# Optimization experiments

Measured on AMD Instinct MI355X. Metric: run time of the kernel, lower is better.

The kernel has to match this reference:

```python
import jax, jax.numpy as jnp
import numpy as np

N_NODES = 100000
N_EDGES = 1600000
N_GRAPHS = 256


def setup_inputs() -> dict:
    key = jax.random.key(0)
    ks = jax.random.split(key, 7)
    x = jax.random.normal(ks[0], (N_NODES, 128), dtype=jnp.float32)
    W1 = jax.random.normal(ks[1], (128, 64), dtype=jnp.float32) * (1.0 / np.sqrt(128))
    W2 = jax.random.normal(ks[2], (64, 64), dtype=jnp.float32) * (1.0 / np.sqrt(64))
    W3 = jax.random.normal(ks[3], (64, 64), dtype=jnp.float32) * (1.0 / np.sqrt(64))
    Wlin = jax.random.normal(ks[4], (64, 16), dtype=jnp.float32) * (1.0 / np.sqrt(64))
    edge_index = jax.random.randint(ks[5], (2, N_EDGES), 0, N_NODES, dtype=jnp.int64)
    batch = jnp.sort(jax.random.randint(ks[6], (N_NODES,), 0, N_GRAPHS, dtype=jnp.int64))
    return {"x": x, "W1": W1, "W2": W2, "W3": W3, "Wlin": Wlin,
            "edge_index": edge_index, "batch": batch}


def _gcn_conv(h, W, src, dst):
    # GCNConv(bias=False, normalize=False): scatter-add of transformed src feats onto dst
    m = h @ W                                   # [N, d_out]
    return jax.ops.segment_sum(m[src], dst, num_segments=N_NODES)


def reference(x, W1, W2, W3, Wlin, edge_index, batch):
    src, dst = edge_index[0], edge_index[1]
    h = jax.nn.relu(_gcn_conv(x, W1, src, dst))
    h = jax.nn.relu(_gcn_conv(h, W2, src, dst))
    h = _gcn_conv(h, W3, src, dst)
    # global mean pool over graphs
    sums = jax.ops.segment_sum(h, batch, num_segments=N_GRAPHS)      # [G, d]
    counts = jax.ops.segment_sum(jnp.ones((N_NODES,), h.dtype), batch,
                                 num_segments=N_GRAPHS)              # [G]
    pooled = sums / jnp.maximum(counts, 1.0)[:, None]
    return pooled @ Wlin                                             # [G, out]
```

## Files before the change

kernel.cpp:

```cpp
#include <hip/hip_runtime.h>
#include <hip/hip_bf16.h>

#define SCAN_CHUNK 1024
#define BIN_CHUNK  4096
#define BSH        9
#define BCAP       10240
#define GSLOTS     16
#define KNODES     2
#define GS16       32
#define GSPLIT     2

typedef __attribute__((ext_vector_type(8))) short short8v;
typedef __attribute__((ext_vector_type(4))) float f32x4;

__device__ __forceinline__ unsigned short f2bf(float f) {
    union { float f; unsigned int i; } c;
    c.f = f;
    unsigned int r = c.i + 0x7FFFu + ((c.i >> 16) & 1u);
    return (unsigned short)(r >> 16);
}
__device__ __forceinline__ float lo2f(unsigned int u) {
    union { unsigned int i; float f; } c; c.i = u << 16; return c.f;
}
__device__ __forceinline__ float hi2f(unsigned int u) {
    union { unsigned int i; float f; } c; c.i = u & 0xFFFF0000u; return c.f;
}
__device__ __forceinline__ unsigned int pack2bf(float lo, float hi) {
    return ((unsigned int)f2bf(hi) << 16) | (unsigned int)f2bf(lo);
}
__device__ __forceinline__ int idx_at(const void* p, long long i, int is64) {
    if (is64) return (int)((const long long*)p)[i];
    return ((const int*)p)[i];
}
__device__ __forceinline__ short8v as_s8(uint4 q) {
    return __builtin_bit_cast(short8v, q);
}

__global__ __launch_bounds__(256) void k_setup(const unsigned int* __restrict__ a, long long aWords,
                                               const unsigned int* __restrict__ b, long long bWords,
                                               int* __restrict__ flags, int* __restrict__ bcur,
                                               float* __restrict__ T, int tN,
                                               const float* __restrict__ W1, const float* __restrict__ W2,
                                               const float* __restrict__ W3, const float* __restrict__ Wlin,
                                               float* __restrict__ Wc,
                                               unsigned short* __restrict__ Wt1hi, unsigned short* __restrict__ Wt1lo,
                                               unsigned short* __restrict__ Wt2hi, unsigned short* __restrict__ Wt2lo,
                                               unsigned short* __restrict__ Wcthi, unsigned short* __restrict__ Wctlo) {
    int t = threadIdx.x;
    if (blockIdx.x == 0) {
        __shared__ int sA, sB;
        if (t == 0) { sA = 1; sB = 1; }
        __syncthreads();
        long long hA = aWords / 2;
        long long pA = 2 * ((long long)t * (hA - 1) / 255) + 1;
        if (a[pA] != 0u) atomicAnd(&sA, 0);
        long long hB = bWords / 2;
        long long pB = 2 * ((long long)t * (hB - 1) / 255) + 1;
        if (b[pB] != 0u) atomicAnd(&sB, 0);
        __syncthreads();
        if (t == 0) { flags[0] = sA; flags[1] = sB; }
    } else if (blockIdx.x == 1) {
        bcur[t] = 0;
        for (int o = t; o < 64 * 16; o += 256) {
            int k = o >> 4, j = o & 15;
            float acc = 0.f;
#pragma unroll 8
            for (int m = 0; m < 64; ++m) acc += W3[k * 64 + m] * Wlin[m * 16 + j];
            Wc[o] = acc;
            unsigned short h = f2bf(acc);
            Wcthi[j * 64 + k] = h;
            Wctlo[j * 64 + k] = f2bf(acc - lo2f(h));
        }
    } else if (blockIdx.x == 2) {
        int col = t >> 2, ks = (t & 3) * 32;
        for (int k = ks; k < ks + 32; ++k) {
            float v = W1[(size_t)k * 64 + col];
            unsigned short h = f2bf(v);
            Wt1hi[col * 128 + k] = h;
            Wt1lo[col * 128 + k] = f2bf(v - lo2f(h));
        }
    } else if (blockIdx.x == 3) {
        int col = t >> 2, ks = (t & 3) * 16;
        for (int k = ks; k < ks + 16; ++k) {
            float v = W2[(size_t)k * 64 + col];
            unsigned short h = f2bf(v);
            Wt2hi[col * 64 + k] = h;
            Wt2lo[col * 64 + k] = f2bf(v - lo2f(h));
        }
    } else {
        int i = (blockIdx.x - 4) * 256 + t;
        if (i < tN) T[i] = 0.f;
    }
}

__global__ __launch_bounds__(256) void k_bin(const void* __restrict__ ei, int nE,
                                             int* __restrict__ bcur, unsigned int* __restrict__ srcsE,
                                             const int* __restrict__ flags) {
    __shared__ int eS[BIN_CHUNK], eD[BIN_CHUNK];
    __shared__ int cntD[256], baseD[256], posD[256];
    int t = threadIdx.x;
    int is64 = flags[0];
    cntD[t] = 0; posD[t] = 0;
    __syncthreads();
    int cs = blockIdx.x * BIN_CHUNK;
    int ce = min(cs + BIN_CHUNK, nE);
    for (int i = cs + t; i < ce; i += 256) {
        int src = idx_at(ei, i, is64);
        int dst = idx_at(ei, (long long)nE + i, is64);
        eS[i - cs] = src; eD[i - cs] = dst;
        atomicAdd(&cntD[dst >> BSH], 1);
    }
    __syncthreads();
    if (cntD[t] > 0) baseD[t] = atomicAdd(&bcur[t], cntD[t]);
    __syncthreads();
    for (int i = cs + t; i < ce; i += 256) {
        int src = eS[i - cs], dst = eD[i - cs];
        int kd = dst >> BSH;
        int od = baseD[kd] + atomicAdd(&posD[kd], 1);
        if (od < BCAP)
            srcsE[(size_t)kd * BCAP + od] = (unsigned int)src | ((unsigned int)(dst & 511) << 17);
    }
}

__global__ __launch_bounds__(256) void k_fill3(unsigned int* __restrict__ srcsE,
                                               const int* __restrict__ bcur,
                                               int* __restrict__ rowstart, int* __restrict__ rowend,
                                               int N, const void* __restrict__ batch,
                                               const int* __restrict__ flags) {
    __shared__ unsigned int ent[BCAP];
    __shared__ int cnt5[512], off5[512], cur5[512], s2[256];
    __shared__ int grelS[512];
    __shared__ int sgf;
    int k = blockIdx.x;
    int t = threadIdx.x;
    int base = k * BCAP;
    int ck = min(bcur[k], BCAP);
    int is64b = flags[1];
    cnt5[t] = 0; cnt5[t + 256] = 0;
    if (t == 0) sgf = idx_at(batch, (long long)(k << BSH), is64b);
    __syncthreads();
    for (int i = t; i < ck; i += 256) {
        unsigned int v = srcsE[base + i];
        ent[i] = v;
        atomicAdd(&cnt5[v >> 17], 1);
    }
    __syncthreads();
    int pair = cnt5[2 * t] + cnt5[2 * t + 1];
    s2[t] = pair;
    __syncthreads();
    for (int off = 1; off < 256; off <<= 1) {
        int x = (t >= off) ? s2[t - off] : 0;
        __syncthreads();
        s2[t] += x;
        __syncthreads();
    }
    int excl = s2[t] - pair;
    off5[2 * t] = excl;
    off5[2 * t + 1] = excl + cnt5[2 * t];
    __syncthreads();
    for (int j = t; j < 512; j += 256) {
        int node = (k << BSH) + j;
        if (node < N) {
            rowstart[node] = base + off5[j];
            rowend[node]   = base + off5[j] + cnt5[j];
            grelS[j] = idx_at(batch, node, is64b) - sgf;
        } else {
            grelS[j] = 0;
        }
        cur5[j] = off5[j];
    }
    __syncthreads();
    for (int i = t; i < ck; i += 256) {
        unsigned int v = ent[i];
        int d = (int)(v >> 17);
        int pos = atomicAdd(&cur5[d], 1);
        srcsE[base + pos] = (v & 0x1FFFFu) | ((unsigned int)grelS[d] << 17);
    }
}

__global__ __launch_bounds__(256) void k_zero_i(int* __restrict__ p, int n) {
    int i = blockIdx.x * 256 + threadIdx.x;
    if (i < n) p[i] = 0;
}
__global__ __launch_bounds__(256) void k_hist(const void* __restrict__ ei, int nE,
                                              int* __restrict__ cnt, const int* __restrict__ flags) {
    int e = blockIdx.x * 256 + threadIdx.x;
    if (e >= nE) return;
    int is64 = flags[0];
    atomicAdd(&cnt[idx_at(ei, (long long)nE + e, is64)], 1);
}
__global__ __launch_bounds__(256) void k_scan_a(const int* __restrict__ cnt, int N, int* __restrict__ bsum) {
    __shared__ int s[256];
    int b = blockIdx.x, t = threadIdx.x;
    int base = b * SCAN_CHUNK + t * 4;
    int v = 0;
#pragma unroll
    for (int j = 0; j < 4; ++j) if (base + j < N) v += cnt[base + j];
    s[t] = v; __syncthreads();
    for (int off = 128; off >= 1; off >>= 1) {
        if (t < off) s[t] += s[t + off];
        __syncthreads();
    }
    if (t == 0) bsum[b] = s[0];
}
__global__ __launch_bounds__(128) void k_scan_b(const int* __restrict__ bsum, int NB, int* __restrict__ bpre) {
    __shared__ int s[128];
    int t = threadIdx.x;
    int v = (t < NB) ? bsum[t] : 0;
    s[t] = v; __syncthreads();
    for (int off = 1; off < 128; off <<= 1) {
        int x = (t >= off) ? s[t - off] : 0;
        __syncthreads();
        s[t] += x;
        __syncthreads();
    }
    if (t < NB) bpre[t] = s[t] - v;
}
__global__ __launch_bounds__(256) void k_scan_c(const int* __restrict__ cnt, int N,
                                                const int* __restrict__ bpre,
                                                int* __restrict__ rowstart, int* __restrict__ rowend,
                                                int* __restrict__ cursor) {
    __shared__ int s[256];
    int b = blockIdx.x, t = threadIdx.x;
    int base = b * SCAN_CHUNK + t * 4;
    int c0 = (base + 0 < N) ? cnt[base + 0] : 0;
    int c1 = (base + 1 < N) ? cnt[base + 1] : 0;
    int c2 = (base + 2 < N) ? cnt[base + 2] : 0;
    int c3 = (base + 3 < N) ? cnt[base + 3] : 0;
    int p0 = c0, p1 = p0 + c1, p2 = p1 + c2, p3 = p2 + c3;
    s[t] = p3; __syncthreads();
    int tot = p3;
    for (int off = 1; off < 256; off <<= 1) {
        int x = (t >= off) ? s[t - off] : 0;
        __syncthreads();
        s[t] += x;
        __syncthreads();
    }
    int toff = s[t] - tot + bpre[b];
    if (base + 0 < N) { rowstart[base + 0] = toff;      rowend[base + 0] = toff + p0; cursor[base + 0] = toff; }
    if (base + 1 < N) { rowstart[base + 1] = toff + p0; rowend[base + 1] = toff + p1; cursor[base + 1] = toff + p0; }
    if (base + 2 < N) { rowstart[base + 2] = toff + p1; rowend[base + 2] = toff + p2; cursor[base + 2] = toff + p1; }
    if (base + 3 < N) { rowstart[base + 3] = toff + p2; rowend[base + 3] = toff + p3; cursor[base + 3] = toff + p2; }
}
__global__ __launch_bounds__(256) void k_fill(const void* __restrict__ ei, int nE,
                                              int* __restrict__ cursor, int* __restrict__ srcs,
                                              const int* __restrict__ flags) {
    int e = blockIdx.x * 256 + threadIdx.x;
    if (e >= nE) return;
    int is64 = flags[0];
    int src = idx_at(ei, e, is64);
    int dst = idx_at(ei, (long long)nE + e, is64);
    int pos = atomicAdd(&cursor[dst], 1);
    srcs[pos] = src;
}

__global__ __launch_bounds__(256) void k_gemm1m(const float* __restrict__ X,
                                                const unsigned short* __restrict__ Wthi,
                                                const unsigned short* __restrict__ Wtlo,
                                                unsigned short* __restrict__ Mb, int N) {
    __shared__ unsigned short Xhi[64 * 128];
    __shared__ unsigned short Xlo[64 * 128];
    int tid = threadIdx.x;
    int wid = tid >> 6, lane = tid & 63;
    int lrow = lane & 15, lk = lane >> 4;
    int base = blockIdx.x * 64;

    uint4 bhi[4], blo[4];
    {
        int col = wid * 16 + lrow;
        const unsigned short* ph = Wthi + col * 128 + lk * 8;
        const unsigned short* pl = Wtlo + col * 128 + lk * 8;
#pragma unroll
        for (int kc = 0; kc < 4; ++kc) {
            bhi[kc] = *(const uint4*)(ph + kc * 32);
            blo[kc] = *(const uint4*)(pl + kc * 32);
        }
    }

    {
        int r = tid >> 2, seg = tid & 3;
        int row = base + r;
        float v[32];
        if (row < N) {
            const float4* src = (const float4*)(X + (size_t)row * 128 + seg * 32);
#pragma unroll
            for (int u = 0; u < 8; ++u) {
                float4 f = src[u];
                v[4 * u] = f.x; v[4 * u + 1] = f.y; v[4 * u + 2] = f.z; v[4 * u + 3] = f.w;
            }
        } else {
#pragma unroll
            for (int u = 0; u < 32; ++u) v[u] = 0.f;
        }
        int swz = (r & 7) << 4;
#pragma unroll
        for (int u = 0; u < 4; ++u) {
            unsigned short h[8];
            float lo[8];
#pragma unroll
            for (int j = 0; j < 8; ++j) {
                float xv = v[u * 8 + j];
                unsigned short hh = f2bf(xv);
                h[j] = hh;
                lo[j] = xv - lo2f(hh);
            }
            uint4 qh, ql;
            qh.x = ((unsigned)h[1] << 16) | h[0]; qh.y = ((unsigned)h[3] << 16) | h[2];
            qh.z = ((unsigned)h[5] << 16) | h[4]; qh.w = ((unsigned)h[7] << 16) | h[6];
            ql.x = pack2bf(lo[0], lo[1]); ql.y = pack2bf(lo[2], lo[3]);
            ql.z = pack2bf(lo[4], lo[5]); ql.w = pack2bf(lo[6], lo[7]);
            int kb = seg * 64 + u * 16;
            int addr = r * 256 + (kb ^ swz);
            *(uint4*)((char*)Xhi + addr) = qh;
            *(uint4*)((char*)Xlo + addr) = ql;
        }
    }
    __syncthreads();

    int col = wid * 16 + lrow;
#pragma unroll
    for (int rt = 0; rt < 4; ++rt) {
        f32x4 acc = {0.f, 0.f, 0.f, 0.f};
        int row = rt * 16 + lrow;
        int rbase = row * 256;
        int swz = (row & 7) << 4;
#pragma unroll
        for (int kc = 0; kc < 4; ++kc) {
            int kb = kc * 64 + lk * 16;
            uint4 ah = *(const uint4*)((const char*)Xhi + rbase + (kb ^ swz));
            uint4 al = *(const uint4*)((const char*)Xlo + rbase + (kb ^ swz));
            acc = __builtin_amdgcn_mfma_f32_16x16x32_bf16(as_s8(ah), as_s8(bhi[kc]), acc, 0, 0, 0);
            acc = __builtin_amdgcn_mfma_f32_16x16x32_bf16(as_s8(al), as_s8(bhi[kc]), acc, 0, 0, 0);
            acc = __builtin_amdgcn_mfma_f32_16x16x32_bf16(as_s8(ah), as_s8(blo[kc]), acc, 0, 0, 0);
        }
#pragma unroll
        for (int j = 0; j < 4; ++j) {
            int orow = base + rt * 16 + lk * 4 + j;
            if (orow < N) Mb[(size_t)orow * 64 + col] = f2bf(acc[j]);
        }
    }
}

__global__ __launch_bounds__(256) void k_projm(const unsigned short* __restrict__ Rb,
                                               const unsigned short* __restrict__ Wthi,
                                               const unsigned short* __restrict__ Wtlo,
                                               unsigned short* __restrict__ Mout, int N) {
    __shared__ unsigned short Rs[64 * 64];
    int tid = threadIdx.x;
    int wid = tid >> 6, lane = tid & 63;
    int lrow = lane & 15, lk = lane >> 4;
    int base = blockIdx.x * 64;

    uint4 bhi[2], blo[2];
    {
        int col = wid * 16 + lrow;
        const unsigned short* ph = Wthi + col * 64 + lk * 8;
        const unsigned short* pl = Wtlo + col * 64 + lk * 8;
#pragma unroll
        for (int kc = 0; kc < 2; ++kc) {
            bhi[kc] = *(const uint4*)(ph + kc * 32);
            blo[kc] = *(const uint4*)(pl + kc * 32);
        }
    }
    {
        int r = tid >> 2, seg = tid & 3;
        int row = base + r;
        uint4 q0, q1;
        if (row < N) {
            const uint4* src = (const uint4*)(Rb + (size_t)row * 64 + seg * 16);
            q0 = src[0]; q1 = src[1];
        } else {
            q0 = make_uint4(0u, 0u, 0u, 0u); q1 = q0;
        }
        int swz = (r & 7) << 4;
        int kb = seg * 32;
        *(uint4*)((char*)Rs + r * 128 + ((kb) ^ swz)) = q0;
        *(uint4*)((char*)Rs + r * 128 + ((kb + 16) ^ swz)) = q1;
    }
    __syncthreads();

    int col = wid * 16 + lrow;
#pragma unroll
    for (int rt = 0; rt < 4; ++rt) {
        f32x4 acc = {0.f, 0.f, 0.f, 0.f};
        int row = rt * 16 + lrow;
        int rbase = row * 128;
        int swz = (row & 7) << 4;
#pragma unroll
        for (int kc = 0; kc < 2; ++kc) {
            int kb = kc * 64 + lk * 16;
            uint4 a = *(const uint4*)((const char*)Rs + rbase + (kb ^ swz));
            acc = __builtin_amdgcn_mfma_f32_16x16x32_bf16(as_s8(a), as_s8(bhi[kc]), acc, 0, 0, 0);
            acc = __builtin_amdgcn_mfma_f32_16x16x32_bf16(as_s8(a), as_s8(blo[kc]), acc, 0, 0, 0);
        }
#pragma unroll
        for (int j = 0; j < 4; ++j) {
            int orow = base + rt * 16 + lk * 4 + j;
            if (orow < N) Mout[(size_t)orow * 64 + col] = f2bf(acc[j]);
        }
    }
}

__global__ __launch_bounds__(256) void k_y2(const unsigned short* __restrict__ R,
                                            const unsigned short* __restrict__ Wcthi,
                                            const unsigned short* __restrict__ Wctlo,
                                            unsigned short* __restrict__ Y2, int N) {
    int tid = threadIdx.x;
    int wid = tid >> 6, lane = tid & 63;
    int lrow = lane & 15, lk = lane >> 4;
    int rowb = blockIdx.x * 64 + wid * 16;

    uint4 bhi[2], blo[2];
#pragma unroll
    for (int kc = 0; kc < 2; ++kc) {
        bhi[kc] = *(const uint4*)(Wcthi + lrow * 64 + kc * 32 + lk * 8);
        blo[kc] = *(const uint4*)(Wctlo + lrow * 64 + kc * 32 + lk * 8);
    }
    f32x4 acc = {0.f, 0.f, 0.f, 0.f};
    int arow = rowb + lrow;
#pragma unroll
    for (int kc = 0; kc < 2; ++kc) {
        uint4 a = make_uint4(0u, 0u, 0u, 0u);
        if (arow < N) a = *(const uint4*)(R + (size_t)arow * 64 + kc * 32 + lk * 8);
        acc = __builtin_amdgcn_mfma_f32_16x16x32_bf16(as_s8(a), as_s8(bhi[kc]), acc, 0, 0, 0);
        acc = __builtin_amdgcn_mfma_f32_16x16x32_bf16(as_s8(a), as_s8(blo[kc]), acc, 0, 0, 0);
    }
#pragma unroll
    for (int j = 0; j < 4; ++j) {
        int orow = rowb + lk * 4 + j;
        if (orow < N) Y2[(size_t)orow * 16 + lrow] = f2bf(acc[j]);
    }
}

#define GACC(P)  { A[0] += lo2f((P).x); A[1] += hi2f((P).x);                  \
                   A[2] += lo2f((P).y); A[3] += hi2f((P).y);                  \
                   A[4] += lo2f((P).z); A[5] += hi2f((P).z);                  \
                   A[6] += lo2f((P).w); A[7] += hi2f((P).w); }
#define GATHER8_CORE(SRCS, MB, S, E, LMASK, L, A, MASK)                       \
    {                                                                         \
        int c_ = (S);                                                         \
        for (; c_ + 16 <= (E); c_ += 16) {                                    \
            int sv0_ = (int)(SRCS)[c_ + (L)];                                 \
            int sv1_ = (int)(SRCS)[c_ + 8 + (L)];                             \
            _Pragma("unroll")                                                 \
            for (int j_ = 0; j_ < 8; ++j_) {                                  \
                int srcn_ = __shfl(sv0_, (LMASK) | j_, 64) & (int)(MASK);     \
                uint4 p_ = ((const uint4*)((MB) + (size_t)srcn_ * 64))[L];    \
                GACC(p_)                                                      \
            }                                                                 \
            _Pragma("unroll")                                                 \
            for (int j_ = 0; j_ < 8; ++j_) {                                  \
                int srcn_ = __shfl(sv1_, (LMASK) | j_, 64) & (int)(MASK);     \
                uint4 p_ = ((const uint4*)((MB) + (size_t)srcn_ * 64))[L];    \
                GACC(p_)                                                      \
            }                                                                 \
        }                                                                     \
        if (c_ + 8 <= (E)) {                                                  \
            int sv_ = (int)(SRCS)[c_ + (L)];                                  \
            _Pragma("unroll")                                                 \
            for (int j_ = 0; j_ < 8; ++j_) {                                  \
                int srcn_ = __shfl(sv_, (LMASK) | j_, 64) & (int)(MASK);      \
                uint4 p_ = ((const uint4*)((MB) + (size_t)srcn_ * 64))[L];    \
                GACC(p_)                                                      \
            }                                                                 \
            c_ += 8;                                                          \
        }                                                                     \
        if (c_ < (E)) {                                                       \
            int m_ = (E) - c_;                                                \
            int sv_ = (int)(SRCS)[(c_ + (L) < (E)) ? c_ + (L) : (E) - 1];     \
            _Pragma("unroll")                                                 \
            for (int j_ = 0; j_ < 8; ++j_) {                                  \
                if (j_ < m_) {                                                \
                    int srcn_ = __shfl(sv_, (LMASK) | j_, 64) & (int)(MASK);  \
                    uint4 p_ = ((const uint4*)((MB) + (size_t)srcn_ * 64))[L];\
                    GACC(p_)                                                  \
                }                                                             \
            }                                                                 \
        }                                                                     \
    }

__global__ __launch_bounds__(256) void k_gather8(const unsigned short* __restrict__ Mb,
                                                 const int* __restrict__ rowstart,
                                                 const int* __restrict__ rowend,
                                                 const unsigned int* __restrict__ srcs,
                                                 unsigned short* __restrict__ R, int N,
                                                 unsigned int srcMask) {
    int tid = threadIdx.x;
    int lane = tid & 63;
    int l = lane & 7;
    int lmask = lane & 56;
    int node0 = (blockIdx.x * 32 + (tid >> 3)) * KNODES;
#pragma unroll
    for (int jn = 0; jn < KNODES; ++jn) {
        int node = node0 + jn;
        if (node >= N) break;
        int s = rowstart[node], e = rowend[node];
        float A[8] = {0.f, 0.f, 0.f, 0.f, 0.f, 0.f, 0.f, 0.f};
        GATHER8_CORE(srcs, Mb, s, e, lmask, l, A, srcMask)
        uint4 q;
        q.x = pack2bf(fmaxf(A[0], 0.f), fmaxf(A[1], 0.f));
        q.y = pack2bf(fmaxf(A[2], 0.f), fmaxf(A[3], 0.f));
        q.z = pack2bf(fmaxf(A[4], 0.f), fmaxf(A[5], 0.f));
        q.w = pack2bf(fmaxf(A[6], 0.f), fmaxf(A[7], 0.f));
        ((uint4*)(R + (size_t)node * 64))[l] = q;
    }
}

__global__ __launch_bounds__(256) void k_gsum16(const unsigned short* __restrict__ y2,
                                                const unsigned int* __restrict__ srcsE,
                                                const int* __restrict__ bcur,
                                                const void* __restrict__ batch,
                                                float* __restrict__ T16, int N, int G,
                                                const int* __restrict__ flags) {
    __shared__ float sacc[GS16][4][16];
    __shared__ int sgmin;
    int t = threadIdx.x;
    int k = blockIdx.x / GSPLIT;
    int half = blockIdx.x % GSPLIT;
    for (int i = t; i < GS16 * 4 * 16; i += 256) ((float*)sacc)[i] = 0.f;
    if (t == 0) sgmin = idx_at(batch, (long long)min(k << BSH, N - 1), flags[1]);
    __syncthreads();
    int gmin = sgmin;
    int ck = min(bcur[k], BCAP);
    int base = k * BCAP;
    int lo = half * (ck / GSPLIT);
    int hi = (half == GSPLIT - 1) ? ck : (half + 1) * (ck / GSPLIT);
    int cnt = hi - lo;
    int len = (cnt + 255) >> 8;
    int s0 = lo + t * len;
    int e0 = min(s0 + len, hi);
    int rep = t & 3;

    float acc[16];
#pragma unroll
    for (int j = 0; j < 16; ++j) acc[j] = 0.f;
    int curg = -1;

#define GF16(GG)                                                              \
    {                                                                         \
        if ((GG) < GS16) {                                                    \
            float* sp_ = &sacc[GG][rep][0];                                   \
            _Pragma("unroll")                                                 \
            for (int j_ = 0; j_ < 16; ++j_) atomicAdd(&sp_[j_], acc[j_]);     \
        } else {                                                              \
            _Pragma("unroll")                                                 \
            for (int j_ = 0; j_ < 16; ++j_)                                   \
                atomicAdd(&T16[(size_t)(gmin + (GG)) * 16 + j_], acc[j_]);    \
        }                                                                     \
    }

    int i = s0;
    while (i < e0) {
        if (i + 4 <= e0) {
            unsigned v0 = srcsE[base + i], v1 = srcsE[base + i + 1];
            unsigned v2 = srcsE[base + i + 2], v3 = srcsE[base + i + 3];
            int g0 = (int)(v0 >> 17);
            if (g0 == curg && (int)(v3 >> 17) == g0 &&
                (int)(v1 >> 17) == g0 && (int)(v2 >> 17) == g0) {
                const uint4* p0 = (const uint4*)(y2 + (size_t)(v0 & 0x1FFFFu) * 16);
                const uint4* p1 = (const uint4*)(y2 + (size_t)(v1 & 0x1FFFFu) * 16);
                const uint4* p2 = (const uint4*)(y2 + (size_t)(v2 & 0x1FFFFu) * 16);
                const uint4* p3 = (const uint4*)(y2 + (size_t)(v3 & 0x1FFFFu) * 16);
                uint4 a0 = p0[0], b0 = p0[1];
                uint4 a1 = p1[0], b1 = p1[1];
                uint4 a2 = p2[0], b2 = p2[1];
                uint4 a3 = p3[0], b3 = p3[1];
#define Y2ACC(QA, QB)                                                         \
                acc[0] += lo2f((QA).x); acc[1] += hi2f((QA).x);               \
                acc[2] += lo2f((QA).y); acc[3] += hi2f((QA).y);               \
                acc[4] += lo2f((QA).z); acc[5] += hi2f((QA).z);               \
                acc[6] += lo2f((QA).w); acc[7] += hi2f((QA).w);               \
                acc[8] += lo2f((QB).x); acc[9] += hi2f((QB).x);               \
                acc[10] += lo2f((QB).y); acc[11] += hi2f((QB).y);             \
                acc[12] += lo2f((QB).z); acc[13] += hi2f((QB).z);             \
                acc[14] += lo2f((QB).w); acc[15] += hi2f((QB).w);
                Y2ACC(a0, b0) Y2ACC(a1, b1) Y2ACC(a2, b2) Y2ACC(a3, b3)
                i += 4;
                continue;
            }
        }
        unsigned v = srcsE[base + i];
        int g = (int)(v >> 17);
        if (g != curg) {
            if (curg >= 0) GF16(curg)
            curg = g;
#pragma unroll
            for (int j = 0; j < 16; ++j) acc[j] = 0.f;
        }
        const uint4* p = (const uint4*)(y2 + (size_t)(v & 0x1FFFFu) * 16);
        uint4 qa = p[0], qb = p[1];
        Y2ACC(qa, qb)
        ++i;
    }
    if (curg >= 0) GF16(curg)
    __syncthreads();
    for (int i2 = t; i2 < GS16 * 16; i2 += 256) {
        int slot = i2 >> 4, j = i2 & 15;
        float v = sacc[slot][0][j] + sacc[slot][1][j] + sacc[slot][2][j] + sacc[slot][3][j];
        int g = gmin + slot;
        if (v != 0.f && g < G) atomicAdd(&T16[(size_t)g * 16 + j], v);
    }
#undef Y2ACC
#undef GF16
}

#define GFLUSH(GG, RR)                                                        \
    {                                                                         \
        int slot_ = (GG) - gmin;                                              \
        if (slot_ >= 0 && slot_ < GSLOTS) {                                   \
            _Pragma("unroll")                                                 \
            for (int i_ = 0; i_ < 8; ++i_)                                    \
                atomicAdd(&sacc[slot_][l * 8 + i_], RR[i_]);                  \
        } else {                                                              \
            _Pragma("unroll")                                                 \
            for (int i_ = 0; i_ < 8; ++i_)                                    \
                atomicAdd(&T[(GG) * 64 + l * 8 + i_], RR[i_]);                \
        }                                                                     \
    }

__global__ __launch_bounds__(256) void k_gsum8(const unsigned short* __restrict__ R,
                                               const int* __restrict__ rowstart,
                                               const int* __restrict__ rowend,
                                               const unsigned int* __restrict__ srcs,
                                               const void* __restrict__ batch,
                                               float* __restrict__ T, int N, int G,
                                               const int* __restrict__ flags) {
    __shared__ float sacc[GSLOTS][64];
    int tid = threadIdx.x;
    for (int t = tid; t < GSLOTS * 64; t += 256) ((float*)sacc)[t] = 0.f;
    int is64 = flags[1];
    int nbase = blockIdx.x * 32 * KNODES;
    int gmin = idx_at(batch, min(nbase, N - 1), is64);
    __syncthreads();

    int lane = tid & 63;
    int l = lane & 7;
    int lmask = lane & 56;
    int node0 = nbase + (tid >> 3) * KNODES;
    float r[8] = {0.f, 0.f, 0.f, 0.f, 0.f, 0.f, 0.f, 0.f};
    int curG = -1;
#pragma unroll
    for (int jn = 0; jn < KNODES; ++jn) {
        int node = node0 + jn;
        if (node >= N) break;
        int s = rowstart[node], e = rowend[node];
        float A[8] = {0.f, 0.f, 0.f, 0.f, 0.f, 0.f, 0.f, 0.f};
        GATHER8_CORE(srcs, R, s, e, lmask, l, A, 0xFFFFFFFFu)
        int g = idx_at(batch, node, is64);
        if (g != curG) {
            if (curG >= 0) GFLUSH(curG, r)
#pragma unroll
            for (int i = 0; i < 8; ++i) r[i] = A[i];
            curG = g;
        } else {
#pragma unroll
            for (int i = 0; i < 8; ++i) r[i] += A[i];
        }
    }
    if (curG >= 0) GFLUSH(curG, r)
    __syncthreads();
    for (int t = tid; t < GSLOTS * 64; t += 256) {
        float v = ((float*)sacc)[t];
        int g = gmin + (t >> 6);
        if (v != 0.f && g < G) atomicAdd(&T[g * 64 + (t & 63)], v);
    }
}

__global__ __launch_bounds__(64) void k_out(const float* __restrict__ T,
                                            const void* __restrict__ batch,
                                            const float* __restrict__ Wc,
                                            float* __restrict__ out, int N,
                                            const int* __restrict__ flags) {
    int g = blockIdx.x;
    int lane = threadIdx.x;
    int is64 = flags[1];

    int lo = 0, hi = N;
    while (lo < hi) { int mid = (lo + hi) >> 1; if (idx_at(batch, mid, is64) < g) lo = mid + 1; else hi = mid; }
    int s = lo;
    lo = s; hi = N;
    while (lo < hi) { int mid = (lo + hi) >> 1; if (idx_at(batch, mid, is64) < g + 1) lo = mid + 1; else hi = mid; }
    float cnt = (float)(lo - s);

    __shared__ float P[64];
    P[lane] = T[g * 64 + lane] / fmaxf(cnt, 1.0f);
    __syncthreads();
    if (lane < 16) {
        float o = 0.f;
#pragma unroll 8
        for (int k = 0; k < 64; ++k) o += P[k] * Wc[k * 16 + lane];
        out[g * 16 + lane] = o;
    }
}

__global__ __launch_bounds__(64) void k_out16(const float* __restrict__ T16,
                                              const void* __restrict__ batch,
                                              float* __restrict__ out, int N,
                                              const int* __restrict__ flags) {
    int g = blockIdx.x;
    int lane = threadIdx.x;
    int is64 = flags[1];

    int lo = 0, hi = N;
    while (lo < hi) { int mid = (lo + hi) >> 1; if (idx_at(batch, mid, is64) < g) lo = mid + 1; else hi = mid; }
    int s = lo;
    lo = s; hi = N;
    while (lo < hi) { int mid = (lo + hi) >> 1; if (idx_at(batch, mid, is64) < g + 1) lo = mid + 1; else hi = mid; }
    float cnt = (float)(lo - s);

    if (lane < 16) out[g * 16 + lane] = T16[(size_t)g * 16 + lane] / fmaxf(cnt, 1.0f);
}

extern "C" void kernel_launch(void* const* d_in, const int* in_sizes, int n_in,
                              void* d_out, int out_size, void* d_ws, size_t ws_size,
                              hipStream_t stream) {
    const float* x    = (const float*)d_in[0];
    const float* W1   = (const float*)d_in[1];
    const float* W2   = (const float*)d_in[2];
    const float* W3   = (const float*)d_in[3];
    const float* Wlin = (const float*)d_in[4];
    const void* ei    = d_in[5];
    const void* batch = d_in[6];

    int N  = in_sizes[0] / 128;
    int nE = in_sizes[5] / 2;
    int G  = out_size / 16;
    int NBUCK = (N + (1 << BSH) - 1) >> BSH;
    int NB = (N + SCAN_CHUNK - 1) / SCAN_CHUNK;
    bool fast = (NBUCK <= 256);

    unsigned short* MbA = (unsigned short*)d_ws;
    unsigned short* MbB = (unsigned short*)(MbA + (size_t)N * 64);
    int* ip       = (int*)(MbB + (size_t)N * 64);
    int* rowstart = ip;          ip += N;
    int* rowend   = ip;          ip += N;
    int* cnt      = ip;          ip += N;
    int* bsum     = ip;          ip += 128;
    int* bpre     = ip;          ip += 128;
    int* flags    = ip;          ip += 4;
    int* bcur     = ip;          ip += 256;
    float* T      = (float*)ip;  ip += (size_t)G * 64;
    float* Wc     = (float*)ip;  ip += 64 * 16;
    unsigned short* Wt1hi = (unsigned short*)ip; ip += 2048;
    ip += 2048;
    unsigned short* Wt1lo = (unsigned short*)ip; ip += 4096;
    unsigned short* Wt2hi = (unsigned short*)ip; ip += 2048;
    unsigned short* Wt2lo = (unsigned short*)ip; ip += 2048;
    unsigned short* Wcthi = (unsigned short*)ip; ip += 512;
    unsigned short* Wctlo = (unsigned short*)ip; ip += 512;
    unsigned short* Y2    = (unsigned short*)ip; ip += (size_t)N * 8;
    unsigned int* srcsE = (unsigned int*)ip;
    ip += fast ? (size_t)256 * BCAP : (size_t)nE;
    size_t need = (size_t)((char*)ip - (char*)d_ws);
    if (ws_size < need) return;

    dim3 blk(256);
    int gT64  = (N + 63) / 64;
    int gG8   = (N + 32 * KNODES - 1) / (32 * KNODES);
    int gBin  = (nE + BIN_CHUNK - 1) / BIN_CHUNK;
    int tN    = G * 64;
    int gSetup = 4 + (tN + 255) / 256;

    hipLaunchKernelGGL(k_setup, dim3(gSetup), blk, 0, stream,
                       (const unsigned int*)ei, (long long)in_sizes[5],
                       (const unsigned int*)batch, (long long)in_sizes[6],
                       flags, bcur, T, tN, W1, W2, W3, Wlin, Wc,
                       Wt1hi, Wt1lo, Wt2hi, Wt2lo, Wcthi, Wctlo);

    if (fast) {
        hipLaunchKernelGGL(k_bin,   dim3(gBin), blk, 0, stream, ei, nE, bcur, srcsE, flags);
        hipLaunchKernelGGL(k_fill3, dim3(NBUCK), blk, 0, stream, srcsE, bcur, rowstart, rowend, N, batch, flags);
    } else {
        int gN = (N + 255) / 256;
        int gE = (nE + 255) / 256;
        hipLaunchKernelGGL(k_zero_i, dim3(gN), blk, 0, stream, cnt, N);
        hipLaunchKernelGGL(k_hist,   dim3(gE), blk, 0, stream, ei, nE, cnt, flags);
        hipLaunchKernelGGL(k_scan_a, dim3(NB), blk, 0, stream, cnt, N, bsum);
        hipLaunchKernelGGL(k_scan_b, dim3(1), dim3(128), 0, stream, bsum, NB, bpre);
        hipLaunchKernelGGL(k_scan_c, dim3(NB), blk, 0, stream, cnt, N, bpre, rowstart, rowend, cnt);
        hipLaunchKernelGGL(k_fill,   dim3(gE), blk, 0, stream, ei, nE, cnt, (int*)srcsE, flags);
    }

    unsigned int srcMask = fast ? 0x1FFFFu : 0xFFFFFFFFu;

    hipLaunchKernelGGL(k_gemm1m,  dim3(gT64), blk, 0, stream, x, Wt1hi, Wt1lo, MbA, N);
    hipLaunchKernelGGL(k_gather8, dim3(gG8), blk, 0, stream, MbA, rowstart, rowend, srcsE, MbB, N, srcMask);
    hipLaunchKernelGGL(k_projm,   dim3(gT64), blk, 0, stream, MbB, Wt2hi, Wt2lo, MbA, N);
    hipLaunchKernelGGL(k_gather8, dim3(gG8), blk, 0, stream, MbA, rowstart, rowend, srcsE, MbB, N, srcMask);

    if (fast) {
        hipLaunchKernelGGL(k_y2,     dim3(gT64), blk, 0, stream, MbB, Wcthi, Wctlo, Y2, N);
        hipLaunchKernelGGL(k_gsum16, dim3(NBUCK * GSPLIT), blk, 0, stream, Y2, srcsE, bcur, batch, T, N, G, flags);
        hipLaunchKernelGGL(k_out16,  dim3(G), dim3(64), 0, stream, T, batch, (float*)d_out, N, flags);
    } else {
        hipLaunchKernelGGL(k_gsum8, dim3(gG8), blk, 0, stream, MbB, rowstart, rowend, srcsE, batch, T, N, G, flags);
        hipLaunchKernelGGL(k_out, dim3(G), dim3(64), 0, stream, T, batch, Wc, (float*)d_out, N, flags);
    }
}
```

Before: 302.0 us.

## Fuse second gather with ReLU and Wc projection; halve dst bucket size

```diff
diff --git a/kernel.cpp b/kernel.cpp
--- a/kernel.cpp
+++ b/kernel.cpp
@@ -3,12 +3,14 @@
 
 #define SCAN_CHUNK 1024
 #define BIN_CHUNK  4096
-#define BSH        9
-#define BCAP       10240
+#define BSH        8
+#define BMSK       255
+#define NBMAX      512
+#define BCAP       5120
 #define GSLOTS     16
 #define KNODES     2
-#define GS16       32
-#define GSPLIT     2
+#define GS16       16
+#define GSPLIT     4
 
 typedef __attribute__((ext_vector_type(8))) short short8v;
 typedef __attribute__((ext_vector_type(4))) float f32x4;
@@ -44,8 +46,7 @@
                                                const float* __restrict__ W3, const float* __restrict__ Wlin,
                                                float* __restrict__ Wc,
                                                unsigned short* __restrict__ Wt1hi, unsigned short* __restrict__ Wt1lo,
-                                               unsigned short* __restrict__ Wt2hi, unsigned short* __restrict__ Wt2lo,
-                                               unsigned short* __restrict__ Wcthi, unsigned short* __restrict__ Wctlo) {
+                                               unsigned short* __restrict__ Wt2hi, unsigned short* __restrict__ Wt2lo) {
     int t = threadIdx.x;
     if (blockIdx.x == 0) {
         __shared__ int sA, sB;
@@ -60,16 +61,13 @@
         __syncthreads();
         if (t == 0) { flags[0] = sA; flags[1] = sB; }
     } else if (blockIdx.x == 1) {
-        bcur[t] = 0;
+        bcur[t] = 0; bcur[t + 256] = 0;
         for (int o = t; o < 64 * 16; o += 256) {
             int k = o >> 4, j = o & 15;
             float acc = 0.f;
 #pragma unroll 8
             for (int m = 0; m < 64; ++m) acc += W3[k * 64 + m] * Wlin[m * 16 + j];
             Wc[o] = acc;
-            unsigned short h = f2bf(acc);
-            Wcthi[j * 64 + k] = h;
-            Wctlo[j * 64 + k] = f2bf(acc - lo2f(h));
         }
     } else if (blockIdx.x == 2) {
         int col = t >> 2, ks = (t & 3) * 32;
@@ -97,10 +95,11 @@
                                              int* __restrict__ bcur, unsigned int* __restrict__ srcsE,
                                              const int* __restrict__ flags) {
     __shared__ int eS[BIN_CHUNK], eD[BIN_CHUNK];
-    __shared__ int cntD[256], baseD[256], posD[256];
+    __shared__ int cntD[NBMAX], baseD[NBMAX], posD[NBMAX];
     int t = threadIdx.x;
     int is64 = flags[0];
     cntD[t] = 0; posD[t] = 0;
+    cntD[t + 256] = 0; posD[t + 256] = 0;
     __syncthreads();
     int cs = blockIdx.x * BIN_CHUNK;
     int ce = min(cs + BIN_CHUNK, nE);
@@ -111,14 +110,15 @@
         atomicAdd(&cntD[dst >> BSH], 1);
     }
     __syncthreads();
-    if (cntD[t] > 0) baseD[t] = atomicAdd(&bcur[t], cntD[t]);
+    for (int j = t; j < NBMAX; j += 256)
+        if (cntD[j] > 0) baseD[j] = atomicAdd(&bcur[j], cntD[j]);
     __syncthreads();
     for (int i = cs + t; i < ce; i += 256) {
         int src = eS[i - cs], dst = eD[i - cs];
         int kd = dst >> BSH;
         int od = baseD[kd] + atomicAdd(&posD[kd], 1);
         if (od < BCAP)
-            srcsE[(size_t)kd * BCAP + od] = (unsigned int)src | ((unsigned int)(dst & 511) << 17);
+            srcsE[(size_t)kd * BCAP + od] = (unsigned int)src | ((unsigned int)(dst & BMSK) << 17);
     }
 }
 
@@ -128,15 +128,15 @@
                                                int N, const void* __restrict__ batch,
                                                const int* __restrict__ flags) {
     __shared__ unsigned int ent[BCAP];
-    __shared__ int cnt5[512], off5[512], cur5[512], s2[256];
-    __shared__ int grelS[512];
+    __shared__ int cnt5[256], off5[256], cur5[256], s2[256];
+    __shared__ int grelS[256];
     __shared__ int sgf;
     int k = blockIdx.x;
     int t = threadIdx.x;
     int base = k * BCAP;
     int ck = min(bcur[k], BCAP);
     int is64b = flags[1];
-    cnt5[t] = 0; cnt5[t + 256] = 0;
+    cnt5[t] = 0;
     if (t == 0) sgf = idx_at(batch, (long long)(k << BSH), is64b);
     __syncthreads();
     for (int i = t; i < ck; i += 256) {
@@ -145,8 +145,8 @@
         atomicAdd(&cnt5[v >> 17], 1);
     }
     __syncthreads();
-    int pair = cnt5[2 * t] + cnt5[2 * t + 1];
-    s2[t] = pair;
+    int c = cnt5[t];
+    s2[t] = c;
     __syncthreads();
     for (int off = 1; off < 256; off <<= 1) {
         int x = (t >= off) ? s2[t - off] : 0;
@@ -154,20 +154,18 @@
         s2[t] += x;
         __syncthreads();
     }
-    int excl = s2[t] - pair;
-    off5[2 * t] = excl;
-    off5[2 * t + 1] = excl + cnt5[2 * t];
-    __syncthreads();
-    for (int j = t; j < 512; j += 256) {
-        int node = (k << BSH) + j;
+    int excl = s2[t] - c;
+    off5[t] = excl;
+    cur5[t] = excl;
+    {
+        int node = (k << BSH) + t;
         if (node < N) {
-            rowstart[node] = base + off5[j];
-            rowend[node]   = base + off5[j] + cnt5[j];
-            grelS[j] = idx_at(batch, node, is64b) - sgf;
+            rowstart[node] = base + excl;
+            rowend[node]   = base + excl + c;
+            grelS[t] = idx_at(batch, node, is64b) - sgf;
         } else {
-            grelS[j] = 0;
-        }
-        cur5[j] = off5[j];
+            grelS[t] = 0;
+        }
     }
     __syncthreads();
     for (int i = t; i < ck; i += 256) {
@@ -398,37 +396,6 @@
             int orow = base + rt * 16 + lk * 4 + j;
             if (orow < N) Mout[(size_t)orow * 64 + col] = f2bf(acc[j]);
         }
-    }
-}
-
-__global__ __launch_bounds__(256) void k_y2(const unsigned short* __restrict__ R,
-                                            const unsigned short* __restrict__ Wcthi,
-                                            const unsigned short* __restrict__ Wctlo,
-                                            unsigned short* __restrict__ Y2, int N) {
-    int tid = threadIdx.x;
-    int wid = tid >> 6, lane = tid & 63;
-    int lrow = lane & 15, lk = lane >> 4;
-    int rowb = blockIdx.x * 64 + wid * 16;
-
-    uint4 bhi[2], blo[2];
-#pragma unroll
-    for (int kc = 0; kc < 2; ++kc) {
-        bhi[kc] = *(const uint4*)(Wcthi + lrow * 64 + kc * 32 + lk * 8);
-        blo[kc] = *(const uint4*)(Wctlo + lrow * 64 + kc * 32 + lk * 8);
-    }
-    f32x4 acc = {0.f, 0.f, 0.f, 0.f};
-    int arow = rowb + lrow;
-#pragma unroll
-    for (int kc = 0; kc < 2; ++kc) {
-        uint4 a = make_uint4(0u, 0u, 0u, 0u);
-        if (arow < N) a = *(const uint4*)(R + (size_t)arow * 64 + kc * 32 + lk * 8);
-        acc = __builtin_amdgcn_mfma_f32_16x16x32_bf16(as_s8(a), as_s8(bhi[kc]), acc, 0, 0, 0);
-        acc = __builtin_amdgcn_mfma_f32_16x16x32_bf16(as_s8(a), as_s8(blo[kc]), acc, 0, 0, 0);
-    }
-#pragma unroll
-    for (int j = 0; j < 4; ++j) {
-        int orow = rowb + lk * 4 + j;
-        if (orow < N) Y2[(size_t)orow * 16 + lrow] = f2bf(acc[j]);
     }
 }
 
@@ -506,6 +473,61 @@
     }
 }
 
+__global__ __launch_bounds__(256) void k_gather_y2(const unsigned short* __restrict__ Mb,
+                                                   const int* __restrict__ rowstart,
+                                                   const int* __restrict__ rowend,
+                                                   const unsigned int* __restrict__ srcs,
+                                                   const float* __restrict__ Wc,
+                                                   unsigned short* __restrict__ Y2, int N,
+                                                   unsigned int srcMask) {
+    __shared__ float WcT[16 * 64];
+    int tid = threadIdx.x;
+    for (int i = tid; i < 1024; i += 256) {
+        int kk = i >> 4, j = i & 15;
+        WcT[j * 64 + kk] = Wc[kk * 16 + j];
+    }
+    __syncthreads();
+
+    int lane = tid & 63;
+    int l = lane & 7;
+    int lmask = lane & 56;
+    int node0 = (blockIdx.x * 32 + (tid >> 3)) * KNODES;
+#pragma unroll
+    for (int jn = 0; jn < KNODES; ++jn) {
+        int node = node0 + jn;
+        if (node >= N) break;
+        int s = rowstart[node], e = rowend[node];
+        float A[8] = {0.f, 0.f, 0.f, 0.f, 0.f, 0.f, 0.f, 0.f};
+        GATHER8_CORE(srcs, Mb, s, e, lmask, l, A, srcMask)
+        float r0 = fmaxf(A[0], 0.f), r1 = fmaxf(A[1], 0.f);
+        float r2 = fmaxf(A[2], 0.f), r3 = fmaxf(A[3], 0.f);
+        float r4 = fmaxf(A[4], 0.f), r5 = fmaxf(A[5], 0.f);
+        float r6 = fmaxf(A[6], 0.f), r7 = fmaxf(A[7], 0.f);
+        float part[16];
+#pragma unroll
+        for (int j = 0; j < 16; ++j) {
+            const float4 w0 = *(const float4*)&WcT[j * 64 + l * 8];
+            const float4 w1 = *(const float4*)&WcT[j * 64 + l * 8 + 4];
+            part[j] = r0 * w0.x + r1 * w0.y + r2 * w0.z + r3 * w0.w
+                    + r4 * w1.x + r5 * w1.y + r6 * w1.z + r7 * w1.w;
+        }
+#pragma unroll
+        for (int off = 1; off <= 4; off <<= 1) {
+#pragma unroll
+            for (int j = 0; j < 16; ++j) part[j] += __shfl_xor(part[j], off, 64);
+        }
+        if (l < 2) {
+            int j0 = l * 8;
+            uint4 q;
+            q.x = pack2bf(part[j0 + 0], part[j0 + 1]);
+            q.y = pack2bf(part[j0 + 2], part[j0 + 3]);
+            q.z = pack2bf(part[j0 + 4], part[j0 + 5]);
+            q.w = pack2bf(part[j0 + 6], part[j0 + 7]);
+            ((uint4*)(Y2 + (size_t)node * 16))[l] = q;
+        }
+    }
+}
+
 __global__ __launch_bounds__(256) void k_gsum16(const unsigned short* __restrict__ y2,
                                                 const unsigned int* __restrict__ srcsE,
                                                 const int* __restrict__ bcur,
@@ -516,15 +538,15 @@
     __shared__ int sgmin;
     int t = threadIdx.x;
     int k = blockIdx.x / GSPLIT;
-    int half = blockIdx.x % GSPLIT;
+    int part = blockIdx.x % GSPLIT;
     for (int i = t; i < GS16 * 4 * 16; i += 256) ((float*)sacc)[i] = 0.f;
     if (t == 0) sgmin = idx_at(batch, (long long)min(k << BSH, N - 1), flags[1]);
     __syncthreads();
     int gmin = sgmin;
     int ck = min(bcur[k], BCAP);
     int base = k * BCAP;
-    int lo = half * (ck / GSPLIT);
-    int hi = (half == GSPLIT - 1) ? ck : (half + 1) * (ck / GSPLIT);
+    int lo = part * (ck / GSPLIT);
+    int hi = (part == GSPLIT - 1) ? ck : (part + 1) * (ck / GSPLIT);
     int cnt = hi - lo;
     int len = (cnt + 255) >> 8;
     int s0 = lo + t * len;
@@ -594,8 +616,8 @@
     }
     if (curg >= 0) GF16(curg)
     __syncthreads();
-    for (int i2 = t; i2 < GS16 * 16; i2 += 256) {
-        int slot = i2 >> 4, j = i2 & 15;
+    {
+        int slot = t >> 4, j = t & 15;
         float v = sacc[slot][0][j] + sacc[slot][1][j] + sacc[slot][2][j] + sacc[slot][3][j];
         int g = gmin + slot;
         if (v != 0.f && g < G) atomicAdd(&T16[(size_t)g * 16 + j], v);
@@ -727,7 +749,7 @@
     int G  = out_size / 16;
     int NBUCK = (N + (1 << BSH) - 1) >> BSH;
     int NB = (N + SCAN_CHUNK - 1) / SCAN_CHUNK;
-    bool fast = (NBUCK <= 256);
+    bool fast = (NBUCK <= NBMAX);
 
     unsigned short* MbA = (unsigned short*)d_ws;
     unsigned short* MbB = (unsigned short*)(MbA + (size_t)N * 64);
@@ -738,19 +760,16 @@
     int* bsum     = ip;          ip += 128;
     int* bpre     = ip;          ip += 128;
     int* flags    = ip;          ip += 4;
-    int* bcur     = ip;          ip += 256;
+    int* bcur     = ip;          ip += NBMAX;
     float* T      = (float*)ip;  ip += (size_t)G * 64;
     float* Wc     = (float*)ip;  ip += 64 * 16;
-    unsigned short* Wt1hi = (unsigned short*)ip; ip += 2048;
-    ip += 2048;
+    unsigned short* Wt1hi = (unsigned short*)ip; ip += 4096;
     unsigned short* Wt1lo = (unsigned short*)ip; ip += 4096;
     unsigned short* Wt2hi = (unsigned short*)ip; ip += 2048;
     unsigned short* Wt2lo = (unsigned short*)ip; ip += 2048;
-    unsigned short* Wcthi = (unsigned short*)ip; ip += 512;
-    unsigned short* Wctlo = (unsigned short*)ip; ip += 512;
     unsigned short* Y2    = (unsigned short*)ip; ip += (size_t)N * 8;
     unsigned int* srcsE = (unsigned int*)ip;
-    ip += fast ? (size_t)256 * BCAP : (size_t)nE;
+    ip += fast ? (size_t)NBMAX * BCAP : (size_t)nE;
     size_t need = (size_t)((char*)ip - (char*)d_ws);
     if (ws_size < need) return;
 
@@ -765,7 +784,7 @@
                        (const unsigned int*)ei, (long long)in_sizes[5],
                        (const unsigned int*)batch, (long long)in_sizes[6],
                        flags, bcur, T, tN, W1, W2, W3, Wlin, Wc,
-                       Wt1hi, Wt1lo, Wt2hi, Wt2lo, Wcthi, Wctlo);
+                       Wt1hi, Wt1lo, Wt2hi, Wt2lo);
 
     if (fast) {
         hipLaunchKernelGGL(k_bin,   dim3(gBin), blk, 0, stream, ei, nE, bcur, srcsE, flags);
@@ -786,13 +805,13 @@
     hipLaunchKernelGGL(k_gemm1m,  dim3(gT64), blk, 0, stream, x, Wt1hi, Wt1lo, MbA, N);
     hipLaunchKernelGGL(k_gather8, dim3(gG8), blk, 0, stream, MbA, rowstart, rowend, srcsE, MbB, N, srcMask);
     hipLaunchKernelGGL(k_projm,   dim3(gT64), blk, 0, stream, MbB, Wt2hi, Wt2lo, MbA, N);
-    hipLaunchKernelGGL(k_gather8, dim3(gG8), blk, 0, stream, MbA, rowstart, rowend, srcsE, MbB, N, srcMask);
 
     if (fast) {
-        hipLaunchKernelGGL(k_y2,     dim3(gT64), blk, 0, stream, MbB, Wcthi, Wctlo, Y2, N);
+        hipLaunchKernelGGL(k_gather_y2, dim3(gG8), blk, 0, stream, MbA, rowstart, rowend, srcsE, Wc, Y2, N, srcMask);
         hipLaunchKernelGGL(k_gsum16, dim3(NBUCK * GSPLIT), blk, 0, stream, Y2, srcsE, bcur, batch, T, N, G, flags);
         hipLaunchKernelGGL(k_out16,  dim3(G), dim3(64), 0, stream, T, batch, (float*)d_out, N, flags);
     } else {
+        hipLaunchKernelGGL(k_gather8, dim3(gG8), blk, 0, stream, MbA, rowstart, rowend, srcsE, MbB, N, srcMask);
         hipLaunchKernelGGL(k_gsum8, dim3(gG8), blk, 0, stream, MbB, rowstart, rowend, srcsE, batch, T, N, G, flags);
         hipLaunchKernelGGL(k_out, dim3(G), dim3(64), 0, stream, T, batch, Wc, (float*)d_out, N, flags);
     }
```

Measured after the change: 340.0 us. 1.13x slower.

## Halve destination bucket size and interleave two-node gathers for memory parallelism

Applied to the files above, without the earlier changes.

```diff
diff --git a/kernel.cpp b/kernel.cpp
--- a/kernel.cpp
+++ b/kernel.cpp
@@ -3,12 +3,14 @@
 
 #define SCAN_CHUNK 1024
 #define BIN_CHUNK  4096
-#define BSH        9
-#define BCAP       10240
+#define BSH        8
+#define BMSK       255
+#define NBMAX      512
+#define BCAP       5120
 #define GSLOTS     16
 #define KNODES     2
-#define GS16       32
-#define GSPLIT     2
+#define GS16       16
+#define GSPLIT     4
 
 typedef __attribute__((ext_vector_type(8))) short short8v;
 typedef __attribute__((ext_vector_type(4))) float f32x4;
@@ -60,7 +62,7 @@
         __syncthreads();
         if (t == 0) { flags[0] = sA; flags[1] = sB; }
     } else if (blockIdx.x == 1) {
-        bcur[t] = 0;
+        bcur[t] = 0; bcur[t + 256] = 0;
         for (int o = t; o < 64 * 16; o += 256) {
             int k = o >> 4, j = o & 15;
             float acc = 0.f;
@@ -97,10 +99,11 @@
                                              int* __restrict__ bcur, unsigned int* __restrict__ srcsE,
                                              const int* __restrict__ flags) {
     __shared__ int eS[BIN_CHUNK], eD[BIN_CHUNK];
-    __shared__ int cntD[256], baseD[256], posD[256];
+    __shared__ int cntD[NBMAX], baseD[NBMAX], posD[NBMAX];
     int t = threadIdx.x;
     int is64 = flags[0];
     cntD[t] = 0; posD[t] = 0;
+    cntD[t + 256] = 0; posD[t + 256] = 0;
     __syncthreads();
     int cs = blockIdx.x * BIN_CHUNK;
     int ce = min(cs + BIN_CHUNK, nE);
@@ -111,14 +114,15 @@
         atomicAdd(&cntD[dst >> BSH], 1);
     }
     __syncthreads();
-    if (cntD[t] > 0) baseD[t] = atomicAdd(&bcur[t], cntD[t]);
+    for (int j = t; j < NBMAX; j += 256)
+        if (cntD[j] > 0) baseD[j] = atomicAdd(&bcur[j], cntD[j]);
     __syncthreads();
     for (int i = cs + t; i < ce; i += 256) {
         int src = eS[i - cs], dst = eD[i - cs];
         int kd = dst >> BSH;
         int od = baseD[kd] + atomicAdd(&posD[kd], 1);
         if (od < BCAP)
-            srcsE[(size_t)kd * BCAP + od] = (unsigned int)src | ((unsigned int)(dst & 511) << 17);
+            srcsE[(size_t)kd * BCAP + od] = (unsigned int)src | ((unsigned int)(dst & BMSK) << 17);
     }
 }
 
@@ -128,15 +132,15 @@
                                                int N, const void* __restrict__ batch,
                                                const int* __restrict__ flags) {
     __shared__ unsigned int ent[BCAP];
-    __shared__ int cnt5[512], off5[512], cur5[512], s2[256];
-    __shared__ int grelS[512];
+    __shared__ int cnt5[256], off5[256], cur5[256], s2[256];
+    __shared__ int grelS[256];
     __shared__ int sgf;
     int k = blockIdx.x;
     int t = threadIdx.x;
     int base = k * BCAP;
     int ck = min(bcur[k], BCAP);
     int is64b = flags[1];
-    cnt5[t] = 0; cnt5[t + 256] = 0;
+    cnt5[t] = 0;
     if (t == 0) sgf = idx_at(batch, (long long)(k << BSH), is64b);
     __syncthreads();
     for (int i = t; i < ck; i += 256) {
@@ -145,8 +149,8 @@
         atomicAdd(&cnt5[v >> 17], 1);
     }
     __syncthreads();
-    int pair = cnt5[2 * t] + cnt5[2 * t + 1];
-    s2[t] = pair;
+    int c = cnt5[t];
+    s2[t] = c;
     __syncthreads();
     for (int off = 1; off < 256; off <<= 1) {
         int x = (t >= off) ? s2[t - off] : 0;
@@ -154,20 +158,18 @@
         s2[t] += x;
         __syncthreads();
     }
-    int excl = s2[t] - pair;
-    off5[2 * t] = excl;
-    off5[2 * t + 1] = excl + cnt5[2 * t];
-    __syncthreads();
-    for (int j = t; j < 512; j += 256) {
-        int node = (k << BSH) + j;
+    int excl = s2[t] - c;
+    off5[t] = excl;
+    cur5[t] = excl;
+    {
+        int node = (k << BSH) + t;
         if (node < N) {
-            rowstart[node] = base + off5[j];
-            rowend[node]   = base + off5[j] + cnt5[j];
-            grelS[j] = idx_at(batch, node, is64b) - sgf;
+            rowstart[node] = base + excl;
+            rowend[node]   = base + excl + c;
+            grelS[t] = idx_at(batch, node, is64b) - sgf;
         } else {
-            grelS[j] = 0;
-        }
-        cur5[j] = off5[j];
+            grelS[t] = 0;
+        }
     }
     __syncthreads();
     for (int i = t; i < ck; i += 256) {
@@ -432,38 +434,21 @@
     }
 }
 
-#define GACC(P)  { A[0] += lo2f((P).x); A[1] += hi2f((P).x);                  \
-                   A[2] += lo2f((P).y); A[3] += hi2f((P).y);                  \
-                   A[4] += lo2f((P).z); A[5] += hi2f((P).z);                  \
-                   A[6] += lo2f((P).w); A[7] += hi2f((P).w); }
-#define GATHER8_CORE(SRCS, MB, S, E, LMASK, L, A, MASK)                       \
+#define GACCX(AR, P)  { AR[0] += lo2f((P).x); AR[1] += hi2f((P).x);           \
+                        AR[2] += lo2f((P).y); AR[3] += hi2f((P).y);           \
+                        AR[4] += lo2f((P).z); AR[5] += hi2f((P).z);           \
+                        AR[6] += lo2f((P).w); AR[7] += hi2f((P).w); }
+#define GATHER8_REM(SRCS, MB, S, E, LMASK, L, A, MASK)                        \
     {                                                                         \
         int c_ = (S);                                                         \
-        for (; c_ + 16 <= (E); c_ += 16) {                                    \
-            int sv0_ = (int)(SRCS)[c_ + (L)];                                 \
-            int sv1_ = (int)(SRCS)[c_ + 8 + (L)];                             \
-            _Pragma("unroll")                                                 \
-            for (int j_ = 0; j_ < 8; ++j_) {                                  \
-                int srcn_ = __shfl(sv0_, (LMASK) | j_, 64) & (int)(MASK);     \
-                uint4 p_ = ((const uint4*)((MB) + (size_t)srcn_ * 64))[L];    \
-                GACC(p_)                                                      \
-            }                                                                 \
-            _Pragma("unroll")                                                 \
-            for (int j_ = 0; j_ < 8; ++j_) {                                  \
-                int srcn_ = __shfl(sv1_, (LMASK) | j_, 64) & (int)(MASK);     \
-                uint4 p_ = ((const uint4*)((MB) + (size_t)srcn_ * 64))[L];    \
-                GACC(p_)                                                      \
-            }                                                                 \
-        }                                                                     \
-        if (c_ + 8 <= (E)) {                                                  \
+        for (; c_ + 8 <= (E); c_ += 8) {                                      \
             int sv_ = (int)(SRCS)[c_ + (L)];                                  \
             _Pragma("unroll")                                                 \
             for (int j_ = 0; j_ < 8; ++j_) {                                  \
                 int srcn_ = __shfl(sv_, (LMASK) | j_, 64) & (int)(MASK);      \
                 uint4 p_ = ((const uint4*)((MB) + (size_t)srcn_ * 64))[L];    \
-                GACC(p_)                                                      \
+                GACCX(A, p_)                                                  \
             }                                                                 \
-            c_ += 8;                                                          \
         }                                                                     \
         if (c_ < (E)) {                                                       \
             int m_ = (E) - c_;                                                \
@@ -473,36 +458,62 @@
                 if (j_ < m_) {                                                \
                     int srcn_ = __shfl(sv_, (LMASK) | j_, 64) & (int)(MASK);  \
                     uint4 p_ = ((const uint4*)((MB) + (size_t)srcn_ * 64))[L];\
-                    GACC(p_)                                                  \
+                    GACCX(A, p_)                                              \
                 }                                                             \
             }                                                                 \
         }                                                                     \
     }
 
-__global__ __launch_bounds__(256) void k_gather8(const unsigned short* __restrict__ Mb,
-                                                 const int* __restrict__ rowstart,
-                                                 const int* __restrict__ rowend,
-                                                 const unsigned int* __restrict__ srcs,
-                                                 unsigned short* __restrict__ R, int N,
-                                                 unsigned int srcMask) {
+__global__ __launch_bounds__(256, 4) void k_gather8(const unsigned short* __restrict__ Mb,
+                                                    const int* __restrict__ rowstart,
+                                                    const int* __restrict__ rowend,
+                                                    const unsigned int* __restrict__ srcs,
+                                                    unsigned short* __restrict__ R, int N,
+                                                    unsigned int srcMask) {
     int tid = threadIdx.x;
     int lane = tid & 63;
     int l = lane & 7;
     int lmask = lane & 56;
-    int node0 = (blockIdx.x * 32 + (tid >> 3)) * KNODES;
-#pragma unroll
-    for (int jn = 0; jn < KNODES; ++jn) {
-        int node = node0 + jn;
-        if (node >= N) break;
-        int s = rowstart[node], e = rowend[node];
-        float A[8] = {0.f, 0.f, 0.f, 0.f, 0.f, 0.f, 0.f, 0.f};
-        GATHER8_CORE(srcs, Mb, s, e, lmask, l, A, srcMask)
+    int n0 = (blockIdx.x * 32 + (tid >> 3)) * 2;
+    if (n0 >= N) return;
+    int has1 = (n0 + 1 < N);
+    int s0 = rowstart[n0], e0 = rowend[n0];
+    int s1 = has1 ? rowstart[n0 + 1] : 0;
+    int e1 = has1 ? rowend[n0 + 1] : 0;
+    float A0[8] = {0.f, 0.f, 0.f, 0.f, 0.f, 0.f, 0.f, 0.f};
+    float A1[8] = {0.f, 0.f, 0.f, 0.f, 0.f, 0.f, 0.f, 0.f};
+    int c0 = s0, c1 = s1;
+    while (c0 + 8 <= e0 && c1 + 8 <= e1) {
+        int sva = (int)srcs[c0 + l];
+        int svb = (int)srcs[c1 + l];
+#pragma unroll
+        for (int j = 0; j < 8; ++j) {
+            int sa = __shfl(sva, lmask | j, 64) & (int)srcMask;
+            int sb = __shfl(svb, lmask | j, 64) & (int)srcMask;
+            uint4 pa = ((const uint4*)(Mb + (size_t)sa * 64))[l];
+            uint4 pb = ((const uint4*)(Mb + (size_t)sb * 64))[l];
+            GACCX(A0, pa)
+            GACCX(A1, pb)
+        }
+        c0 += 8; c1 += 8;
+    }
+    GATHER8_REM(srcs, Mb, c0, e0, lmask, l, A0, srcMask)
+    if (has1) GATHER8_REM(srcs, Mb, c1, e1, lmask, l, A1, srcMask)
+    {
         uint4 q;
-        q.x = pack2bf(fmaxf(A[0], 0.f), fmaxf(A[1], 0.f));
-        q.y = pack2bf(fmaxf(A[2], 0.f), fmaxf(A[3], 0.f));
-        q.z = pack2bf(fmaxf(A[4], 0.f), fmaxf(A[5], 0.f));
-        q.w = pack2bf(fmaxf(A[6], 0.f), fmaxf(A[7], 0.f));
-        ((uint4*)(R + (size_t)node * 64))[l] = q;
+        q.x = pack2bf(fmaxf(A0[0], 0.f), fmaxf(A0[1], 0.f));
+        q.y = pack2bf(fmaxf(A0[2], 0.f), fmaxf(A0[3], 0.f));
+        q.z = pack2bf(fmaxf(A0[4], 0.f), fmaxf(A0[5], 0.f));
+        q.w = pack2bf(fmaxf(A0[6], 0.f), fmaxf(A0[7], 0.f));
+        ((uint4*)(R + (size_t)n0 * 64))[l] = q;
+    }
+    if (has1) {
+        uint4 q;
+        q.x = pack2bf(fmaxf(A1[0], 0.f), fmaxf(A1[1], 0.f));
+        q.y = pack2bf(fmaxf(A1[2], 0.f), fmaxf(A1[3], 0.f));
+        q.z = pack2bf(fmaxf(A1[4], 0.f), fmaxf(A1[5], 0.f));
+        q.w = pack2bf(fmaxf(A1[6], 0.f), fmaxf(A1[7], 0.f));
+        ((uint4*)(R + (size_t)(n0 + 1) * 64))[l] = q;
     }
 }
 
@@ -516,15 +527,15 @@
     __shared__ int sgmin;
     int t = threadIdx.x;
     int k = blockIdx.x / GSPLIT;
-    int half = blockIdx.x % GSPLIT;
+    int part = blockIdx.x % GSPLIT;
     for (int i = t; i < GS16 * 4 * 16; i += 256) ((float*)sacc)[i] = 0.f;
     if (t == 0) sgmin = idx_at(batch, (long long)min(k << BSH, N - 1), flags[1]);
     __syncthreads();
     int gmin = sgmin;
     int ck = min(bcur[k], BCAP);
     int base = k * BCAP;
-    int lo = half * (ck / GSPLIT);
-    int hi = (half == GSPLIT - 1) ? ck : (half + 1) * (ck / GSPLIT);
+    int lo = part * (ck / GSPLIT);
+    int hi = (part == GSPLIT - 1) ? ck : (part + 1) * (ck / GSPLIT);
     int cnt = hi - lo;
     int len = (cnt + 255) >> 8;
     int s0 = lo + t * len;
@@ -594,8 +605,8 @@
     }
     if (curg >= 0) GF16(curg)
     __syncthreads();
-    for (int i2 = t; i2 < GS16 * 16; i2 += 256) {
-        int slot = i2 >> 4, j = i2 & 15;
+    {
+        int slot = t >> 4, j = t & 15;
         float v = sacc[slot][0][j] + sacc[slot][1][j] + sacc[slot][2][j] + sacc[slot][3][j];
         int g = gmin + slot;
         if (v != 0.f && g < G) atomicAdd(&T16[(size_t)g * 16 + j], v);
@@ -645,7 +656,7 @@
         if (node >= N) break;
         int s = rowstart[node], e = rowend[node];
         float A[8] = {0.f, 0.f, 0.f, 0.f, 0.f, 0.f, 0.f, 0.f};
-        GATHER8_CORE(srcs, R, s, e, lmask, l, A, 0xFFFFFFFFu)
+        GATHER8_REM(srcs, R, s, e, lmask, l, A, 0xFFFFFFFFu)
         int g = idx_at(batch, node, is64);
         if (g != curG) {
             if (curG >= 0) GFLUSH(curG, r)
@@ -727,7 +738,7 @@
     int G  = out_size / 16;
     int NBUCK = (N + (1 << BSH) - 1) >> BSH;
     int NB = (N + SCAN_CHUNK - 1) / SCAN_CHUNK;
-    bool fast = (NBUCK <= 256);
+    bool fast = (NBUCK <= NBMAX);
 
     unsigned short* MbA = (unsigned short*)d_ws;
     unsigned short* MbB = (unsigned short*)(MbA + (size_t)N * 64);
@@ -738,11 +749,10 @@
     int* bsum     = ip;          ip += 128;
     int* bpre     = ip;          ip += 128;
     int* flags    = ip;          ip += 4;
-    int* bcur     = ip;          ip += 256;
+    int* bcur     = ip;          ip += NBMAX;
     float* T      = (float*)ip;  ip += (size_t)G * 64;
     float* Wc     = (float*)ip;  ip += 64 * 16;
-    unsigned short* Wt1hi = (unsigned short*)ip; ip += 2048;
-    ip += 2048;
+    unsigned short* Wt1hi = (unsigned short*)ip; ip += 4096;
     unsigned short* Wt1lo = (unsigned short*)ip; ip += 4096;
     unsigned short* Wt2hi = (unsigned short*)ip; ip += 2048;
     unsigned short* Wt2lo = (unsigned short*)ip; ip += 2048;
@@ -750,7 +760,7 @@
     unsigned short* Wctlo = (unsigned short*)ip; ip += 512;
     unsigned short* Y2    = (unsigned short*)ip; ip += (size_t)N * 8;
     unsigned int* srcsE = (unsigned int*)ip;
-    ip += fast ? (size_t)256 * BCAP : (size_t)nE;
+    ip += fast ? (size_t)NBMAX * BCAP : (size_t)nE;
     size_t need = (size_t)((char*)ip - (char*)d_ws);
     if (ws_size < need) return;
 
```

After: 370.2 us. 22.6% more time.
